# Performance work log

Hardware: AMD Instinct MI355X
Metric: run time of the kernel (lower is better)

## Reference

```python
import jax, jax.numpy as jnp
import numpy as np

B, S, D, H = 4, 1024, 1024, 16
HD = D // H
NEG = 10000.0


def setup_inputs() -> dict:
    key = jax.random.key(0)
    k1, k2, k3 = jax.random.split(key, 3)
    std = 0.02
    return {
        "x": jax.random.normal(k1, (B, S, D), dtype=jnp.float32),
        "mask": jnp.zeros((B, 1, 1, S), dtype=jnp.float32),
        "w_attn": jax.random.normal(k2, (D, 3 * D), dtype=jnp.float32) * std,
        "b_attn": jnp.zeros((1, 3 * D), dtype=jnp.float32),
        "w_proj": jax.random.normal(k3, (D, D), dtype=jnp.float32) * std,
        "b_proj": jnp.zeros((1, D), dtype=jnp.float32),
    }


def reference(x, mask, w_attn, b_attn, w_proj, b_proj):
    b, s, d = x.shape
    # fused QKV projection (Conv1D == dense over last dim)
    qkv = x @ w_attn + b_attn  # [B,S,3D]
    q, k, v = jnp.split(qkv, 3, axis=2)

    def split_heads(t):  # [B,S,D] -> [B,H,S,HD]
        return t.reshape(b, s, H, HD).transpose(0, 2, 1, 3)

    q, k, v = split_heads(q), split_heads(k), split_heads(v)

    w = jnp.einsum("bhqd,bhkd->bhqk", q, k) / jnp.sqrt(jnp.float32(HD))
    # causal mask (lower triangle from lower-right corner)
    i = jnp.arange(s)[:, None]
    j = jnp.arange(s)[None, :]
    bmask = (i >= j).astype(w.dtype)[None, None]  # [1,1,S,S]
    w = w * bmask - NEG * (1.0 - bmask)
    w = w + mask
    w = jax.nn.softmax(w, axis=-1)  # attn_dropout is identity at inference
    a = jnp.einsum("bhqk,bhkd->bhqd", w, v)
    a = a.transpose(0, 2, 1, 3).reshape(b, s, d)  # merge heads
    a = a @ w_proj + b_proj  # resid_dropout identity at inference
    return (a, w)
```

## Files before the change

kernel.cpp:

```cpp
#include <hip/hip_runtime.h>
#include <hip/hip_bf16.h>

constexpr int Bb = 4, Ss = 1024, Dd = 1024, Hh = 16;

typedef __attribute__((ext_vector_type(8))) short short8;
typedef __attribute__((ext_vector_type(4))) float f32x4;

static __device__ __forceinline__ ushort f2bf(float f) {
  union { __hip_bfloat16 h; ushort u; } cv;
  cv.h = __float2bfloat16(f);
  return cv.u;
}

static __device__ __forceinline__ void gl_lds16(const ushort* g, ushort* l) {
  __builtin_amdgcn_global_load_lds(
      (const __attribute__((address_space(1))) void*)g,
      (__attribute__((address_space(3))) void*)l, 16, 0, 0);
}

__global__ __launch_bounds__(256) void cast_f32_bf16(
    const float* __restrict__ in, ushort* __restrict__ out) {
  const int i = (blockIdx.x * 256 + threadIdx.x) * 4;
  const float4 v = *(const float4*)&in[i];
  ushort4 o;
  o.x = f2bf(v.x); o.y = f2bf(v.y); o.z = f2bf(v.z); o.w = f2bf(v.w);
  *(ushort4*)&out[i] = o;
}

__global__ __launch_bounds__(256) void transpose_cast(
    const float* __restrict__ in, ushort* __restrict__ out, int R, int C) {
  __shared__ float T[32][33];
  const int c0 = blockIdx.x * 32, r0 = blockIdx.y * 32;
  const int t = threadIdx.x;
  const int r = t >> 3, c4 = (t & 7) * 4;
  const float4 v = *(const float4*)&in[(size_t)(r0 + r) * C + c0 + c4];
  T[r][c4 + 0] = v.x; T[r][c4 + 1] = v.y;
  T[r][c4 + 2] = v.z; T[r][c4 + 3] = v.w;
  __syncthreads();
  const int cc = t >> 3, rr4 = (t & 7) * 4;
  ushort4 o;
  o.x = f2bf(T[rr4 + 0][cc]); o.y = f2bf(T[rr4 + 1][cc]);
  o.z = f2bf(T[rr4 + 2][cc]); o.w = f2bf(T[rr4 + 3][cc]);
  *(ushort4*)&out[(size_t)(c0 + cc) * R + r0 + rr4] = o;
}

template <int BM, int BN, bool OUT_BF16>
__global__ __launch_bounds__(256) void gemm_bt(
    const ushort* __restrict__ A, const ushort* __restrict__ Bt,
    const float* __restrict__ bias, void* __restrict__ Cout,
    int M, int N, int K) {
  constexpr int TM = BM / 32, TN = BN / 32;
  __shared__ ushort As[BM * 32];
  __shared__ ushort Bs[BN * 32];
  const int tid = threadIdx.x;
  const int wv = tid >> 6, lane = tid & 63;
  const int l15 = lane & 15, quad = lane >> 4;
  const int ln4 = lane >> 2, kp = (lane & 3) * 8;
  const int m0 = blockIdx.y * BM, n0 = blockIdx.x * BN;
  const int wrow = (wv >> 1) * (BM / 2), wcol = (wv & 1) * (BN / 2);

  const ushort* Arow = &A[(size_t)(m0 + wv * 16 + ln4) * K + kp];
  const ushort* Brow = &Bt[(size_t)(n0 + wv * 16 + ln4) * K + kp];
  ushort* As_base = &As[wv * 512];
  ushort* Bs_base = &Bs[wv * 512];

  f32x4 acc[TM][TN] = {};

  for (int k0 = 0; k0 < K; k0 += 32) {
#pragma unroll
    for (int u = 0; u < BM / 64; u++)
      gl_lds16(Arow + (size_t)u * 64 * K + k0, As_base + u * 2048);
#pragma unroll
    for (int u = 0; u < BN / 64; u++)
      gl_lds16(Brow + (size_t)u * 64 * K + k0, Bs_base + u * 2048);
    __syncthreads();
    short8 af[TM], bfr[TN];
#pragma unroll
    for (int i = 0; i < TM; i++)
      af[i] = *(const short8*)&As[(wrow + i * 16 + l15) * 32 + quad * 8];
#pragma unroll
    for (int j = 0; j < TN; j++)
      bfr[j] = *(const short8*)&Bs[(wcol + j * 16 + l15) * 32 + quad * 8];
#pragma unroll
    for (int i = 0; i < TM; i++)
#pragma unroll
      for (int j = 0; j < TN; j++)
        acc[i][j] = __builtin_amdgcn_mfma_f32_16x16x32_bf16(af[i], bfr[j],
                                                            acc[i][j], 0, 0, 0);
    __syncthreads();
  }

#pragma unroll
  for (int j = 0; j < TN; j++) {
    const int col = n0 + wcol + j * 16 + l15;
    const float bv = bias[col];
#pragma unroll
    for (int i = 0; i < TM; i++) {
#pragma unroll
      for (int r = 0; r < 4; r++) {
        const int row = m0 + wrow + i * 16 + quad * 4 + r;
        const float v = acc[i][j][r] + bv;
        if (OUT_BF16)
          ((ushort*)Cout)[(size_t)row * N + col] = f2bf(v);
        else
          ((float*)Cout)[(size_t)row * N + col] = v;
      }
    }
  }
}

__global__ __launch_bounds__(256) void vtrans(const ushort* __restrict__ qkvb,
                                              ushort* __restrict__ vt) {
  __shared__ ushort T[64 * 72];
  const int j0 = blockIdx.x * 64, bh = blockIdx.y;
  const int b = bh >> 4, h = bh & 15;
  const int t = threadIdx.x;
#pragma unroll
  for (int u = 0; u < 2; u++) {
    const int idx = t + 256 * u;
    const int row = idx >> 3, p = idx & 7;
    *(uint4*)&T[row * 72 + p * 8] = *(const uint4*)&qkvb[
        (size_t)((b << 10) + j0 + row) * 3072 + 2048 + h * 64 + p * 8];
  }
  __syncthreads();
#pragma unroll
  for (int u = 0; u < 2; u++) {
    const int idx = t + 256 * u;
    const int d = idx >> 3, p = idx & 7;
    ushort tmp[8];
#pragma unroll
    for (int kk = 0; kk < 8; kk++) tmp[kk] = T[(p * 8 + kk) * 72 + d];
    uint4 o;
    __builtin_memcpy(&o, tmp, 16);
    *(uint4*)&vt[((size_t)bh * 64 + d) * 1024 + j0 + p * 8] = o;
  }
}

__global__ __launch_bounds__(256) void attn_mfma(
    const ushort* __restrict__ qkvb,
    const ushort* __restrict__ vt,
    const float* __restrict__ mask,
    float* __restrict__ w_out,
    ushort* __restrict__ ab) {
  constexpr int LDP = 1032;
  __shared__ ushort Ps[16 * LDP];
  __shared__ float PM[16][4];
  __shared__ float PSum[16][4];

  const int qt = blockIdx.x, bh = blockIdx.y;
  const int b = bh >> 4, h = bh & 15;
  const int q0 = qt * 16;
  const int tid = threadIdx.x;
  const int wv = tid >> 6, lane = tid & 63;
  const int l15 = lane & 15, quad = lane >> 4;

  const size_t rowQ = (size_t)((b << 10) + q0 + l15) * 3072 + h * 64;
  const short8 qf0 = *(const short8*)&qkvb[rowQ + quad * 8];
  const short8 qf1 = *(const short8*)&qkvb[rowQ + 32 + quad * 8];

  float sreg[16][4];

#pragma unroll
  for (int i = 0; i < 16; i++) {
    const int j0 = (wv + 4 * i) * 16;
    const int col = j0 + l15;
    const float mv = mask[(b << 10) + col];
    if (j0 <= q0 + 15) {
      const size_t rowK = (size_t)((b << 10) + j0 + l15) * 3072 + 1024 + h * 64;
      const short8 kf0 = *(const short8*)&qkvb[rowK + quad * 8];
      const short8 kf1 = *(const short8*)&qkvb[rowK + 32 + quad * 8];
      f32x4 c = {0.f, 0.f, 0.f, 0.f};
      c = __builtin_amdgcn_mfma_f32_16x16x32_bf16(qf0, kf0, c, 0, 0, 0);
      c = __builtin_amdgcn_mfma_f32_16x16x32_bf16(qf1, kf1, c, 0, 0, 0);
#pragma unroll
      for (int r = 0; r < 4; r++)
        sreg[i][r] =
            (col <= q0 + quad * 4 + r ? c[r] * 0.125f : -10000.0f) + mv;
    } else {
#pragma unroll
      for (int r = 0; r < 4; r++) sreg[i][r] = -10000.0f + mv;
    }
  }

#pragma unroll
  for (int r = 0; r < 4; r++) {
    float m = sreg[0][r];
#pragma unroll
    for (int i = 1; i < 16; i++) m = fmaxf(m, sreg[i][r]);
#pragma unroll
    for (int off = 1; off < 16; off <<= 1) m = fmaxf(m, __shfl_xor(m, off));
    if (l15 == 0) PM[quad * 4 + r][wv] = m;
  }
  __syncthreads();

  float mrow[4];
#pragma unroll
  for (int r = 0; r < 4; r++) {
    const f32x4 pm4 = *(const f32x4*)&PM[quad * 4 + r][0];
    mrow[r] = fmaxf(fmaxf(pm4[0], pm4[1]), fmaxf(pm4[2], pm4[3]));
  }

  float psum[4] = {0.f, 0.f, 0.f, 0.f};
#pragma unroll
  for (int i = 0; i < 16; i++)
#pragma unroll
    for (int r = 0; r < 4; r++) {
      const float e = __expf(fminf(sreg[i][r] - mrow[r], 0.0f));
      sreg[i][r] = e;
      psum[r] += e;
    }
#pragma unroll
  for (int r = 0; r < 4; r++) {
    float s = psum[r];
#pragma unroll
    for (int off = 1; off < 16; off <<= 1) s += __shfl_xor(s, off);
    if (l15 == 0) PSum[quad * 4 + r][wv] = s;
  }
  __syncthreads();

  float inv4[4];
#pragma unroll
  for (int r = 0; r < 4; r++) {
    const f32x4 ps4 = *(const f32x4*)&PSum[quad * 4 + r][0];
    inv4[r] = 1.0f / fmaxf(ps4[0] + ps4[1] + ps4[2] + ps4[3], 1e-30f);
  }

#pragma unroll
  for (int i = 0; i < 16; i++) {
    const int j0 = (wv + 4 * i) * 16;
#pragma unroll
    for (int r = 0; r < 4; r++) {
      const float p = sreg[i][r] * inv4[r];
      w_out[((size_t)(bh << 10) + q0 + quad * 4 + r) * 1024 + j0 + l15] = p;
      Ps[(quad * 4 + r) * LDP + j0 + l15] = f2bf(p);
    }
  }
  __syncthreads();

  f32x4 oacc = {0.f, 0.f, 0.f, 0.f};
  const int nch = (q0 + 16 + 31) >> 5;
  const ushort* vbase = vt + ((size_t)bh * 64 + wv * 16 + l15) * 1024;
  for (int c = 0; c < nch; c++) {
    const int k0 = c * 32;
    const short8 pf = *(const short8*)&Ps[l15 * LDP + k0 + quad * 8];
    const short8 vf = *(const short8*)&vbase[k0 + quad * 8];
    oacc = __builtin_amdgcn_mfma_f32_16x16x32_bf16(pf, vf, oacc, 0, 0, 0);
  }
#pragma unroll
  for (int r = 0; r < 4; r++) {
    ab[(size_t)((b << 10) + q0 + quad * 4 + r) * 1024 + h * 64 + wv * 16 +
       l15] = f2bf(oacc[r]);
  }
}

extern "C" void kernel_launch(void* const* d_in, const int* in_sizes, int n_in,
                              void* d_out, int out_size, void* d_ws,
                              size_t ws_size, hipStream_t stream) {
  const float* x = (const float*)d_in[0];
  const float* mask = (const float*)d_in[1];
  const float* w_attn = (const float*)d_in[2];
  const float* b_attn = (const float*)d_in[3];
  const float* w_proj = (const float*)d_in[4];
  const float* b_proj = (const float*)d_in[5];

  float* out_a = (float*)d_out;
  float* out_w = out_a + (size_t)Bb * Ss * Dd;

  char* ws = (char*)d_ws;
  ushort* xb   = (ushort*)(ws);
  ushort* wta  = (ushort*)(ws + (8u << 20));
  ushort* wtp  = (ushort*)(ws + (14u << 20));
  ushort* qkvb = (ushort*)(ws + (16u << 20));
  ushort* vt   = (ushort*)(ws + (40u << 20));
  ushort* ab   = (ushort*)(ws + (48u << 20));

  cast_f32_bf16<<<(Bb * Ss * Dd) / 1024, 256, 0, stream>>>(x, xb);
  transpose_cast<<<dim3(3 * Dd / 32, Dd / 32), 256, 0, stream>>>(w_attn, wta,
                                                                 Dd, 3 * Dd);
  transpose_cast<<<dim3(Dd / 32, Dd / 32), 256, 0, stream>>>(w_proj, wtp, Dd,
                                                             Dd);
  gemm_bt<128, 128, true><<<dim3(3 * Dd / 128, Bb * Ss / 128), 256, 0,
                            stream>>>(xb, wta, b_attn, qkvb, Bb * Ss, 3 * Dd,
                                      Dd);
  vtrans<<<dim3(Ss / 64, Bb * Hh), 256, 0, stream>>>(qkvb, vt);
  attn_mfma<<<dim3(Ss / 16, Bb * Hh), 256, 0, stream>>>(qkvb, vt, mask, out_w,
                                                        ab);
  gemm_bt<128, 128, false><<<dim3(Dd / 128, Bb * Ss / 128), 256, 0, stream>>>(
      ab, wtp, b_proj, out_a, Bb * Ss, Dd, Dd);
}
```

Before: 475.5 us.

## Process 32 query rows per attention block with 512 threads, swizzle workgroup order

The attention kernel now handles 32 query rows per block using 8 waves, so each loaded K fragment is reused by two query groups, halving K reads per query. Block indices in both the GEMM and attention kernels are remapped so consecutive workgroups are spread across the 8 XCDs, aiming for better L2 locality. The larger block needs twice the LDS (about 66KB), which may limit occupancy. The launch_bounds hint of 4 blocks may also add register pressure.

```diff
diff --git a/kernel.cpp b/kernel.cpp
--- a/kernel.cpp
+++ b/kernel.cpp
@@ -56,7 +56,13 @@
   const int wv = tid >> 6, lane = tid & 63;
   const int l15 = lane & 15, quad = lane >> 4;
   const int ln4 = lane >> 2, kp = (lane & 3) * 8;
-  const int m0 = blockIdx.y * BM, n0 = blockIdx.x * BN;
+
+  const int nwg = gridDim.x * gridDim.y;
+  const int f = blockIdx.y * gridDim.x + blockIdx.x;
+  const int cpx = nwg >> 3;
+  const int swz = (f & 7) * cpx + (f >> 3);
+  const int bx = swz % gridDim.x, by = swz / gridDim.x;
+  const int m0 = by * BM, n0 = bx * BN;
   const int wrow = (wv >> 1) * (BM / 2), wcol = (wv & 1) * (BN / 2);
 
   const ushort* Arow = &A[(size_t)(m0 + wv * 16 + ln4) * K + kp];
@@ -136,120 +142,155 @@
   }
 }
 
-__global__ __launch_bounds__(256) void attn_mfma(
+__global__ __launch_bounds__(512, 4) void attn_mfma(
     const ushort* __restrict__ qkvb,
     const ushort* __restrict__ vt,
     const float* __restrict__ mask,
     float* __restrict__ w_out,
     ushort* __restrict__ ab) {
   constexpr int LDP = 1032;
-  __shared__ ushort Ps[16 * LDP];
-  __shared__ float PM[16][4];
-  __shared__ float PSum[16][4];
-
-  const int qt = blockIdx.x, bh = blockIdx.y;
+  __shared__ ushort Ps[32 * LDP];
+  __shared__ float PM[32][8];
+  __shared__ float PSum[32][8];
+
+  const int f = blockIdx.y * 32 + blockIdx.x;
+  const int swz = (f & 7) * 256 + (f >> 3);
+  const int qt = swz & 31, bh = swz >> 5;
+
   const int b = bh >> 4, h = bh & 15;
-  const int q0 = qt * 16;
+  const int q0 = qt * 32;
   const int tid = threadIdx.x;
   const int wv = tid >> 6, lane = tid & 63;
   const int l15 = lane & 15, quad = lane >> 4;
 
-  const size_t rowQ = (size_t)((b << 10) + q0 + l15) * 3072 + h * 64;
-  const short8 qf0 = *(const short8*)&qkvb[rowQ + quad * 8];
-  const short8 qf1 = *(const short8*)&qkvb[rowQ + 32 + quad * 8];
-
-  float sreg[16][4];
-
-#pragma unroll
-  for (int i = 0; i < 16; i++) {
-    const int j0 = (wv + 4 * i) * 16;
+  short8 qf0[2], qf1[2];
+#pragma unroll
+  for (int g = 0; g < 2; g++) {
+    const size_t rowQ =
+        (size_t)((b << 10) + q0 + g * 16 + l15) * 3072 + h * 64;
+    qf0[g] = *(const short8*)&qkvb[rowQ + quad * 8];
+    qf1[g] = *(const short8*)&qkvb[rowQ + 32 + quad * 8];
+  }
+
+  float sreg[2][8][4];
+
+#pragma unroll
+  for (int i = 0; i < 8; i++) {
+    const int j0 = (wv + 8 * i) * 16;
     const int col = j0 + l15;
     const float mv = mask[(b << 10) + col];
-    if (j0 <= q0 + 15) {
-      const size_t rowK = (size_t)((b << 10) + j0 + l15) * 3072 + 1024 + h * 64;
+    if (j0 <= q0 + 31) {
+      const size_t rowK =
+          (size_t)((b << 10) + j0 + l15) * 3072 + 1024 + h * 64;
       const short8 kf0 = *(const short8*)&qkvb[rowK + quad * 8];
       const short8 kf1 = *(const short8*)&qkvb[rowK + 32 + quad * 8];
-      f32x4 c = {0.f, 0.f, 0.f, 0.f};
-      c = __builtin_amdgcn_mfma_f32_16x16x32_bf16(qf0, kf0, c, 0, 0, 0);
-      c = __builtin_amdgcn_mfma_f32_16x16x32_bf16(qf1, kf1, c, 0, 0, 0);
-#pragma unroll
-      for (int r = 0; r < 4; r++)
-        sreg[i][r] =
-            (col <= q0 + quad * 4 + r ? c[r] * 0.125f : -10000.0f) + mv;
+#pragma unroll
+      for (int g = 0; g < 2; g++) {
+        f32x4 c = {0.f, 0.f, 0.f, 0.f};
+        c = __builtin_amdgcn_mfma_f32_16x16x32_bf16(qf0[g], kf0, c, 0, 0, 0);
+        c = __builtin_amdgcn_mfma_f32_16x16x32_bf16(qf1[g], kf1, c, 0, 0, 0);
+#pragma unroll
+        for (int r = 0; r < 4; r++)
+          sreg[g][i][r] =
+              (col <= q0 + g * 16 + quad * 4 + r ? c[r] * 0.125f : -10000.0f) +
+              mv;
+      }
     } else {
 #pragma unroll
-      for (int r = 0; r < 4; r++) sreg[i][r] = -10000.0f + mv;
-    }
-  }
-
-#pragma unroll
-  for (int r = 0; r < 4; r++) {
-    float m = sreg[0][r];
-#pragma unroll
-    for (int i = 1; i < 16; i++) m = fmaxf(m, sreg[i][r]);
-#pragma unroll
-    for (int off = 1; off < 16; off <<= 1) m = fmaxf(m, __shfl_xor(m, off));
-    if (l15 == 0) PM[quad * 4 + r][wv] = m;
-  }
-  __syncthreads();
-
-  float mrow[4];
-#pragma unroll
-  for (int r = 0; r < 4; r++) {
-    const f32x4 pm4 = *(const f32x4*)&PM[quad * 4 + r][0];
-    mrow[r] = fmaxf(fmaxf(pm4[0], pm4[1]), fmaxf(pm4[2], pm4[3]));
-  }
-
-  float psum[4] = {0.f, 0.f, 0.f, 0.f};
-#pragma unroll
-  for (int i = 0; i < 16; i++)
+      for (int g = 0; g < 2; g++)
+#pragma unroll
+        for (int r = 0; r < 4; r++) sreg[g][i][r] = -10000.0f + mv;
+    }
+  }
+
+#pragma unroll
+  for (int g = 0; g < 2; g++)
 #pragma unroll
     for (int r = 0; r < 4; r++) {
-      const float e = __expf(fminf(sreg[i][r] - mrow[r], 0.0f));
-      sreg[i][r] = e;
-      psum[r] += e;
-    }
-#pragma unroll
-  for (int r = 0; r < 4; r++) {
-    float s = psum[r];
-#pragma unroll
-    for (int off = 1; off < 16; off <<= 1) s += __shfl_xor(s, off);
-    if (l15 == 0) PSum[quad * 4 + r][wv] = s;
-  }
-  __syncthreads();
-
-  float inv4[4];
-#pragma unroll
-  for (int r = 0; r < 4; r++) {
-    const f32x4 ps4 = *(const f32x4*)&PSum[quad * 4 + r][0];
-    inv4[r] = 1.0f / fmaxf(ps4[0] + ps4[1] + ps4[2] + ps4[3], 1e-30f);
-  }
-
-#pragma unroll
-  for (int i = 0; i < 16; i++) {
-    const int j0 = (wv + 4 * i) * 16;
+      float m = sreg[g][0][r];
+#pragma unroll
+      for (int i = 1; i < 8; i++) m = fmaxf(m, sreg[g][i][r]);
+#pragma unroll
+      for (int off = 1; off < 16; off <<= 1) m = fmaxf(m, __shfl_xor(m, off));
+      if (l15 == 0) PM[g * 16 + quad * 4 + r][wv] = m;
+    }
+  __syncthreads();
+
+  float mrow[2][4];
+#pragma unroll
+  for (int g = 0; g < 2; g++)
 #pragma unroll
     for (int r = 0; r < 4; r++) {
-      const float p = sreg[i][r] * inv4[r];
-      w_out[((size_t)(bh << 10) + q0 + quad * 4 + r) * 1024 + j0 + l15] = p;
-      Ps[(quad * 4 + r) * LDP + j0 + l15] = f2bf(p);
-    }
-  }
-  __syncthreads();
-
+      const f32x4 a = *(const f32x4*)&PM[g * 16 + quad * 4 + r][0];
+      const f32x4 c = *(const f32x4*)&PM[g * 16 + quad * 4 + r][4];
+      mrow[g][r] = fmaxf(fmaxf(fmaxf(a[0], a[1]), fmaxf(a[2], a[3])),
+                         fmaxf(fmaxf(c[0], c[1]), fmaxf(c[2], c[3])));
+    }
+
+  float psum[2][4] = {};
+#pragma unroll
+  for (int i = 0; i < 8; i++)
+#pragma unroll
+    for (int g = 0; g < 2; g++)
+#pragma unroll
+      for (int r = 0; r < 4; r++) {
+        const float e = __expf(fminf(sreg[g][i][r] - mrow[g][r], 0.0f));
+        sreg[g][i][r] = e;
+        psum[g][r] += e;
+      }
+#pragma unroll
+  for (int g = 0; g < 2; g++)
+#pragma unroll
+    for (int r = 0; r < 4; r++) {
+      float s = psum[g][r];
+#pragma unroll
+      for (int off = 1; off < 16; off <<= 1) s += __shfl_xor(s, off);
+      if (l15 == 0) PSum[g * 16 + quad * 4 + r][wv] = s;
+    }
+  __syncthreads();
+
+  float inv4[2][4];
+#pragma unroll
+  for (int g = 0; g < 2; g++)
+#pragma unroll
+    for (int r = 0; r < 4; r++) {
+      const f32x4 a = *(const f32x4*)&PSum[g * 16 + quad * 4 + r][0];
+      const f32x4 c = *(const f32x4*)&PSum[g * 16 + quad * 4 + r][4];
+      inv4[g][r] = 1.0f / fmaxf(a[0] + a[1] + a[2] + a[3] + c[0] + c[1] +
+                                    c[2] + c[3],
+                                1e-30f);
+    }
+
+#pragma unroll
+  for (int i = 0; i < 8; i++) {
+    const int j0 = (wv + 8 * i) * 16;
+#pragma unroll
+    for (int g = 0; g < 2; g++)
+#pragma unroll
+      for (int r = 0; r < 4; r++) {
+        const int row = g * 16 + quad * 4 + r;
+        const float p = sreg[g][i][r] * inv4[g][r];
+        w_out[((size_t)(bh << 10) + q0 + row) * 1024 + j0 + l15] = p;
+        Ps[row * LDP + j0 + l15] = f2bf(p);
+      }
+  }
+  __syncthreads();
+
+  const int pw = wv & 3, g = wv >> 2;
   f32x4 oacc = {0.f, 0.f, 0.f, 0.f};
-  const int nch = (q0 + 16 + 31) >> 5;
-  const ushort* vbase = vt + ((size_t)bh * 64 + wv * 16 + l15) * 1024;
+  const int nch = (q0 + g * 16 + 47) >> 5;
+  const ushort* vbase = vt + ((size_t)bh * 64 + pw * 16 + l15) * 1024;
   for (int c = 0; c < nch; c++) {
     const int k0 = c * 32;
-    const short8 pf = *(const short8*)&Ps[l15 * LDP + k0 + quad * 8];
+    const short8 pf =
+        *(const short8*)&Ps[(g * 16 + l15) * LDP + k0 + quad * 8];
     const short8 vf = *(const short8*)&vbase[k0 + quad * 8];
     oacc = __builtin_amdgcn_mfma_f32_16x16x32_bf16(pf, vf, oacc, 0, 0, 0);
   }
 #pragma unroll
   for (int r = 0; r < 4; r++) {
-    ab[(size_t)((b << 10) + q0 + quad * 4 + r) * 1024 + h * 64 + wv * 16 +
-       l15] = f2bf(oacc[r]);
+    ab[(size_t)((b << 10) + q0 + g * 16 + quad * 4 + r) * 1024 + h * 64 +
+       pw * 16 + l15] = f2bf(oacc[r]);
   }
 }
 
@@ -283,7 +324,7 @@
                             stream>>>(xb, wta, b_attn, qkvb, Bb * Ss, 3 * Dd,
                                       Dd);
   vtrans<<<dim3(Ss / 64, Bb * Hh), 256, 0, stream>>>(qkvb, vt);
-  attn_mfma<<<dim3(Ss / 16, Bb * Hh), 256, 0, stream>>>(qkvb, vt, mask, out_w,
+  attn_mfma<<<dim3(Ss / 32, Bb * Hh), 512, 0, stream>>>(qkvb, vt, mask, out_w,
                                                         ab);
   gemm_bt<128, 128, false><<<dim3(Dd / 128, Bb * Ss / 128), 256, 0, stream>>>(
       ab, wtp, b_proj, out_a, Bb * Ss, Dd, Dd);
```

Result: no change. 478.3 us (+0.6%).
